# Optimization experiments

Hardware: AMD Instinct MI355X
Metric: run time of the kernel (lower is better)

Reference implementation:

```python
import jax, jax.numpy as jnp
import numpy as np

B, H, N, C = 16, 64, 128, 256
HID = 1024   # feedforward hidden
C8 = C // 8  # mlp hidden in pos/score MLPs
EPS = 1e-6


def _ln(x, g, b):
    m = jnp.mean(x, axis=-1, keepdims=True)
    v = jnp.mean((x - m) ** 2, axis=-1, keepdims=True)
    return (x - m) / jnp.sqrt(v + EPS) * g + b


def setup_inputs() -> dict:
    key = jax.random.key(0)
    ks = jax.random.split(key, 24)
    s = lambda k, shape, scale=0.05: jax.random.normal(k, shape, dtype=jnp.float32) * scale
    inp = {
        "query_input": jax.random.normal(ks[0], (B, H, C), dtype=jnp.float32),
        "key_input": jax.random.normal(ks[1], (B, H, N, C), dtype=jnp.float32),
        "relative_pos": jax.random.normal(ks[2], (B, H, N, 4), dtype=jnp.float32),
        "visibility_mask": jax.random.randint(ks[3], (B, H, N, 1), 0, 2, dtype=jnp.int32),
        # layernorms
        "ln1_g": jnp.ones((C,), jnp.float32), "ln1_b": jnp.zeros((C,), jnp.float32),
        "ln2_g": jnp.ones((C,), jnp.float32), "ln2_b": jnp.zeros((C,), jnp.float32),
        # attention projections (no bias)
        "Wq": s(ks[4], (C, C)), "Wk": s(ks[5], (C, C)), "Wv": s(ks[6], (C, C)),
        # position MLP: 4 -> C//8 -> C
        "pos_w1": s(ks[7], (4, C8)), "pos_b1": jnp.zeros((C8,), jnp.float32),
        "pos_w2": s(ks[8], (C8, C)), "pos_b2": jnp.zeros((C,), jnp.float32),
        # score MLP: C -> C//8 -> C
        "sc_w1": s(ks[9], (C, C8)), "sc_b1": jnp.zeros((C8,), jnp.float32),
        "sc_w2": s(ks[10], (C8, C)), "sc_b2": jnp.zeros((C,), jnp.float32),
        # output layer
        "Wo": s(ks[11], (C, C)), "bo": jnp.zeros((C,), jnp.float32),
        # feedforward MLP: C -> HID -> C
        "ff_w1": s(ks[12], (C, HID)), "ff_b1": jnp.zeros((HID,), jnp.float32),
        "ff_w2": s(ks[13], (HID, C)), "ff_b2": jnp.zeros((C,), jnp.float32),
    }
    return inp


def reference(query_input, key_input, relative_pos, visibility_mask,
              ln1_g, ln1_b, ln2_g, ln2_b, Wq, Wk, Wv,
              pos_w1, pos_b1, pos_w2, pos_b2,
              sc_w1, sc_b1, sc_w2, sc_b2, Wo, bo,
              ff_w1, ff_b1, ff_w2, ff_b2):
    # --- attention block with pre-norm + residual ---
    x = _ln(query_input, ln1_g, ln1_b)                      # [B,H,C]
    q = x @ Wq                                              # [B,H,C]
    k = key_input @ Wk                                      # [B,H,N,C]
    v = key_input @ Wv                                      # [B,H,N,C]
    pos = jax.nn.relu(relative_pos @ pos_w1 + pos_b1) @ pos_w2 + pos_b2  # [B,H,N,C]
    attn_in = k - q[:, :, None, :] + pos                    # [B,H,N,C]
    aw = jax.nn.relu(attn_in @ sc_w1 + sc_b1) @ sc_w2 + sc_b2  # [B,H,N,C]
    aw = jnp.where(visibility_mask == 0, -1e9, aw)
    aw = jax.nn.softmax(aw, axis=-2)                        # softmax over N
    agg = jnp.sum((v + pos) * aw, axis=2)                   # [B,H,C]
    attn_out = agg @ Wo + bo
    x = attn_out + query_input
    # --- feedforward block with pre-norm + residual ---
    y = _ln(x, ln2_g, ln2_b)
    y = jax.nn.relu(y @ ff_w1 + ff_b1) @ ff_w2 + ff_b2
    return y + x
```

## Files before the change

kernel.cpp:

```cpp
#include <hip/hip_runtime.h>
#include <math.h>

#define NN 128
#define CC 256
#define HIDN 1024
#define KST 264
#define SST 40
#define EPSL 1e-6f

typedef short s16x8 __attribute__((ext_vector_type(8)));
typedef float f32x4 __attribute__((ext_vector_type(4)));

#define WVOFF    0
#define WTOFF    73728
#define SW2OFF   82944
#define WOB_OFF  91136
#define FW1B_OFF 156672
#define FW2B_OFF 418816
#define QT_BYTE_OFF  1361920
#define AGG_BYTE_OFF 1492992

__device__ __forceinline__ unsigned short f2b(float x) {
    unsigned u = __builtin_bit_cast(unsigned, x);
    u += 0x7fffu + ((u >> 16) & 1u);
    return (unsigned short)(u >> 16);
}
__device__ __forceinline__ float b2f(unsigned short s) {
    return __builtin_bit_cast(float, ((unsigned)s) << 16);
}
__device__ __forceinline__ unsigned pack2(float a, float b) {
    return (unsigned)f2b(a) | ((unsigned)f2b(b) << 16);
}

__device__ __forceinline__ float block_sum_256(float v, float* red) {
    #pragma unroll
    for (int off = 32; off > 0; off >>= 1)
        v += __shfl_down(v, off, 64);
    const int wid = threadIdx.x >> 6;
    if ((threadIdx.x & 63) == 0) red[wid] = v;
    __syncthreads();
    float s = red[0] + red[1] + red[2] + red[3];
    __syncthreads();
    return s;
}

__global__ __launch_bounds__(256)
void prep1(const float* __restrict__ Wv, const float* __restrict__ pw2,
           const float* __restrict__ sw2, const float* __restrict__ fw1,
           const float* __restrict__ fw2, const float* __restrict__ Wo,
           unsigned short* __restrict__ ws16)
{
    int e = blockIdx.x * 256 + threadIdx.x;
    unsigned short v[8];
    if (e < 9216) {
        int koct = e >> 8, col = e & 255;
        #pragma unroll
        for (int j = 0; j < 8; ++j) {
            int k = koct * 8 + j;
            float val = (k < 256) ? Wv[k * 256 + col] : pw2[(k - 256) * 256 + col];
            v[j] = f2b(val);
        }
        int dest = WVOFF + (col >> 4) * 4608 + (koct >> 2) * 512
                 + (((((koct & 3) << 4) | (col & 15))) << 3);
        uint4 pk;
        pk.x = (unsigned)v[0] | ((unsigned)v[1] << 16);
        pk.y = (unsigned)v[2] | ((unsigned)v[3] << 16);
        pk.z = (unsigned)v[4] | ((unsigned)v[5] << 16);
        pk.w = (unsigned)v[6] | ((unsigned)v[7] << 16);
        *(uint4*)&ws16[dest] = pk;
    } else if (e < 10240) {
        int i = e - 9216;
        int koct = i & 3, col = i >> 2;
        #pragma unroll
        for (int j = 0; j < 8; ++j) v[j] = f2b(sw2[(koct * 8 + j) * 256 + col]);
        int dest = SW2OFF + (col >> 4) * 512 + ((((koct << 4) | (col & 15))) << 3);
        uint4 pk;
        pk.x = (unsigned)v[0] | ((unsigned)v[1] << 16);
        pk.y = (unsigned)v[2] | ((unsigned)v[3] << 16);
        pk.z = (unsigned)v[4] | ((unsigned)v[5] << 16);
        pk.w = (unsigned)v[6] | ((unsigned)v[7] << 16);
        *(uint4*)&ws16[dest] = pk;
    } else {
        const float* src; int base, i;
        if (e < 43008)      { src = fw1; base = FW1B_OFF; i = (e - 10240) * 8; }
        else if (e < 75776) { src = fw2; base = FW2B_OFF; i = (e - 43008) * 8; }
        else                { src = Wo;  base = WOB_OFF;  i = (e - 75776) * 8; }
        float4 a = *(const float4*)(src + i);
        float4 b = *(const float4*)(src + i + 4);
        uint4 pk;
        pk.x = pack2(a.x, a.y);
        pk.y = pack2(a.z, a.w);
        pk.z = pack2(b.x, b.y);
        pk.w = pack2(b.z, b.w);
        *(uint4*)&ws16[base + i] = pk;
    }
}

__global__ __launch_bounds__(256)
void prep2(const float* __restrict__ Wk, const float* __restrict__ pw2,
           const float* __restrict__ sw1, unsigned short* __restrict__ ws16)
{
    int tid = blockIdx.x * 256 + threadIdx.x;
    int k = tid >> 5, j = tid & 31;
    const float* row = (k < 256) ? (Wk + (size_t)k * 256) : (pw2 + (size_t)(k - 256) * 256);
    float s = 0.0f;
    for (int c = 0; c < 256; ++c) s = fmaf(row[c], sw1[c * 32 + j], s);
    int dest = WTOFF + ((j >> 4) * 9 + (k >> 5)) * 512
             + ((((((k >> 3) & 3) << 4) | (j & 15))) << 3) + (k & 7);
    ws16[dest] = f2b(s);
}

__global__ __launch_bounds__(256)
void qprep(const float* __restrict__ qin,
           const float* __restrict__ ln1g, const float* __restrict__ ln1b,
           const float* __restrict__ Wq, const float* __restrict__ pb2,
           const float* __restrict__ sw1, const float* __restrict__ sb1,
           float* __restrict__ qt)
{
    __shared__ __align__(16) float xlnL[4][CC];
    __shared__ __align__(16) float qmL[4][CC];
    const int t = threadIdx.x;
    const int lane = t & 63;
    const int r = t >> 6;
    const int b0 = blockIdx.x * 4;
    const size_t rowoff = (size_t)(b0 + r) * CC;

    float v0 = qin[rowoff + lane];
    float v1 = qin[rowoff + lane + 64];
    float v2 = qin[rowoff + lane + 128];
    float v3 = qin[rowoff + lane + 192];
    float s = v0 + v1 + v2 + v3;
    #pragma unroll
    for (int off = 32; off > 0; off >>= 1) s += __shfl_xor(s, off);
    float mean = s * (1.0f / CC);
    float d0 = v0 - mean, d1 = v1 - mean, d2 = v2 - mean, d3 = v3 - mean;
    float vs = d0 * d0 + d1 * d1 + d2 * d2 + d3 * d3;
    #pragma unroll
    for (int off = 32; off > 0; off >>= 1) vs += __shfl_xor(vs, off);
    float rstd = rsqrtf(vs * (1.0f / CC) + EPSL);
    xlnL[r][lane]       = d0 * rstd * ln1g[lane] + ln1b[lane];
    xlnL[r][lane + 64]  = d1 * rstd * ln1g[lane + 64] + ln1b[lane + 64];
    xlnL[r][lane + 128] = d2 * rstd * ln1g[lane + 128] + ln1b[lane + 128];
    xlnL[r][lane + 192] = d3 * rstd * ln1g[lane + 192] + ln1b[lane + 192];
    __syncthreads();

    float q0 = 0.f, q1 = 0.f, q2 = 0.f, q3 = 0.f;
    for (int k4 = 0; k4 < CC / 4; ++k4) {
        float4 x0 = *(const float4*)&xlnL[0][k4 * 4];
        float4 x1 = *(const float4*)&xlnL[1][k4 * 4];
        float4 x2 = *(const float4*)&xlnL[2][k4 * 4];
        float4 x3 = *(const float4*)&xlnL[3][k4 * 4];
        const float* w = Wq + (size_t)(k4 * 4) * CC + t;
        float w0 = w[0], w1 = w[CC], w2 = w[2 * CC], w3 = w[3 * CC];
        q0 = fmaf(x0.x, w0, fmaf(x0.y, w1, fmaf(x0.z, w2, fmaf(x0.w, w3, q0))));
        q1 = fmaf(x1.x, w0, fmaf(x1.y, w1, fmaf(x1.z, w2, fmaf(x1.w, w3, q1))));
        q2 = fmaf(x2.x, w0, fmaf(x2.y, w1, fmaf(x2.z, w2, fmaf(x2.w, w3, q2))));
        q3 = fmaf(x3.x, w0, fmaf(x3.y, w1, fmaf(x3.z, w2, fmaf(x3.w, w3, q3))));
    }
    float pb = pb2[t];
    qmL[0][t] = pb - q0;
    qmL[1][t] = pb - q1;
    qmL[2][t] = pb - q2;
    qmL[3][t] = pb - q3;
    __syncthreads();

    if (t < 128) {
        int r2 = t >> 5, j = t & 31;
        float acc = sb1[j];
        for (int c = 0; c < 256; ++c) acc = fmaf(qmL[r2][c], sw1[c * 32 + j], acc);
        qt[(size_t)(b0 + r2) * 32 + j] = acc;
    }
}

__global__ __launch_bounds__(256, 2)
void cft_attn(const float* __restrict__ kin, const float* __restrict__ rel,
              const int* __restrict__ vis,
              const float* __restrict__ pw1, const float* __restrict__ pb1,
              const float* __restrict__ pb2, const float* __restrict__ sb2,
              const unsigned short* __restrict__ ws16,
              const float* __restrict__ qt,
              float* __restrict__ aggout)
{
    __shared__ __align__(16) unsigned char smem[80032];
    unsigned short* keyb = (unsigned short*)smem;
    float* poolA = (float*)(smem + 77824);
    float* poolB = (float*)(smem + 78848);
    unsigned char* visb = smem + 79872;
    float* aggpool = (float*)smem;
    float* lpool   = (float*)(smem + 4096);

    const int bh = blockIdx.x;
    const int t = threadIdx.x;
    const int lane = t & 63;
    const int wvid = t >> 6;
    const int quad = lane >> 4;
    const int l16 = lane & 15;
    const int rb = wvid * 32;
    unsigned short* strip = (unsigned short*)(smem + 67584) + wvid * (32 * SST);

    const float4* kb4 = (const float4*)(kin + (size_t)bh * NN * CC);
    #pragma unroll
    for (int i = 0; i < 32; ++i) {
        int flat = i * 256 + t;
        int row = flat >> 6;
        int cu = flat & 63;
        float4 kv = kb4[flat];
        uint2 pk;
        pk.x = pack2(kv.x, kv.y);
        pk.y = pack2(kv.z, kv.w);
        *(uint2*)&keyb[row * KST + cu * 4] = pk;
    }
    if (t < NN) visb[t] = (unsigned char)(vis[(size_t)bh * NN + t] != 0);
    poolB[t] = pb2[t];

    union { s16x8 v; unsigned short u[8]; } phf0, phf1;
    {
        const int row0 = rb + l16, row1 = rb + 16 + l16;
        float4 r40 = *(const float4*)(rel + ((size_t)bh * NN + row0) * 4);
        float4 r41 = *(const float4*)(rel + ((size_t)bh * NN + row1) * 4);
        #pragma unroll
        for (int j = 0; j < 8; ++j) {
            int col = quad * 8 + j;
            float w0 = pw1[col], w1 = pw1[32 + col], w2 = pw1[64 + col], w3 = pw1[96 + col];
            float b = pb1[col];
            float v0 = fmaf(r40.x, w0, fmaf(r40.y, w1, fmaf(r40.z, w2, fmaf(r40.w, w3, b))));
            float v1 = fmaf(r41.x, w0, fmaf(r41.y, w1, fmaf(r41.z, w2, fmaf(r41.w, w3, b))));
            phf0.u[j] = f2b(fmaxf(v0, 0.0f));
            phf1.u[j] = f2b(fmaxf(v1, 0.0f));
        }
    }
    const float qt0 = qt[(size_t)bh * 32 + l16];
    const float qt1 = qt[(size_t)bh * 32 + 16 + l16];
    __syncthreads();

    const int aoff0 = (rb + l16) * KST;
    const int aoff1 = (rb + 16 + l16) * KST;
    const unsigned short* wsv = ws16 + WVOFF;
    const unsigned short* wst = ws16 + WTOFF;
    const unsigned short* ws2 = ws16 + SW2OFF;

    unsigned char vm[2][4];
    #pragma unroll
    for (int mt = 0; mt < 2; ++mt)
        #pragma unroll
        for (int r = 0; r < 4; ++r) vm[mt][r] = visb[rb + mt * 16 + quad * 4 + r];

    f32x4 hacc[2][2];
    #pragma unroll
    for (int mt = 0; mt < 2; ++mt)
        #pragma unroll
        for (int jt = 0; jt < 2; ++jt) hacc[mt][jt] = (f32x4){0.f, 0.f, 0.f, 0.f};
    #pragma unroll
    for (int kt = 0; kt < 8; ++kt) {
        s16x8 A0 = *(const s16x8*)&keyb[aoff0 + kt * 32 + quad * 8];
        s16x8 A1 = *(const s16x8*)&keyb[aoff1 + kt * 32 + quad * 8];
        #pragma unroll
        for (int jt = 0; jt < 2; ++jt) {
            s16x8 B = *(const s16x8*)(wst + (size_t)(jt * 9 + kt) * 512 + lane * 8);
            hacc[0][jt] = __builtin_amdgcn_mfma_f32_16x16x32_bf16(A0, B, hacc[0][jt], 0, 0, 0);
            hacc[1][jt] = __builtin_amdgcn_mfma_f32_16x16x32_bf16(A1, B, hacc[1][jt], 0, 0, 0);
        }
    }
    #pragma unroll
    for (int jt = 0; jt < 2; ++jt) {
        s16x8 B = *(const s16x8*)(wst + (size_t)(jt * 9 + 8) * 512 + lane * 8);
        hacc[0][jt] = __builtin_amdgcn_mfma_f32_16x16x32_bf16(phf0.v, B, hacc[0][jt], 0, 0, 0);
        hacc[1][jt] = __builtin_amdgcn_mfma_f32_16x16x32_bf16(phf1.v, B, hacc[1][jt], 0, 0, 0);
    }
    #pragma unroll
    for (int mt = 0; mt < 2; ++mt)
        #pragma unroll
        for (int jt = 0; jt < 2; ++jt) {
            float qv = jt ? qt1 : qt0;
            int rw = (mt * 16 + quad * 4) * SST + jt * 16 + l16;
            strip[rw]           = f2b(fmaxf(hacc[mt][jt][0] + qv, 0.0f));
            strip[rw + SST]     = f2b(fmaxf(hacc[mt][jt][1] + qv, 0.0f));
            strip[rw + 2 * SST] = f2b(fmaxf(hacc[mt][jt][2] + qv, 0.0f));
            strip[rw + 3 * SST] = f2b(fmaxf(hacc[mt][jt][3] + qv, 0.0f));
        }

    s16x8 H0 = *(const s16x8*)&strip[l16 * SST + quad * 8];
    s16x8 H1 = *(const s16x8*)&strip[(16 + l16) * SST + quad * 8];
    float mloc[16];
    #pragma unroll
    for (int ct = 0; ct < 16; ++ct) {
        f32x4 a0 = (f32x4){0.f, 0.f, 0.f, 0.f};
        f32x4 a1 = (f32x4){0.f, 0.f, 0.f, 0.f};
        s16x8 B = *(const s16x8*)(ws2 + ((size_t)ct * 64 + lane) * 8);
        a0 = __builtin_amdgcn_mfma_f32_16x16x32_bf16(H0, B, a0, 0, 0, 0);
        a1 = __builtin_amdgcn_mfma_f32_16x16x32_bf16(H1, B, a1, 0, 0, 0);
        float sb2c = sb2[ct * 16 + l16];
        float ml = -3.0e38f;
        #pragma unroll
        for (int r = 0; r < 4; ++r) {
            float s0 = vm[0][r] ? (a0[r] + sb2c) : -1e9f;
            float s1 = vm[1][r] ? (a1[r] + sb2c) : -1e9f;
            ml = fmaxf(ml, fmaxf(s0, s1));
        }
        ml = fmaxf(ml, __shfl_xor(ml, 16));
        ml = fmaxf(ml, __shfl_xor(ml, 32));
        mloc[ct] = ml;
    }
    __syncthreads();
    #pragma unroll 1
    for (int w = 0; w < 4; ++w) {
        if (wvid == w && lane < 16) {
            #pragma unroll
            for (int ct = 0; ct < 16; ++ct) {
                int x = ct * 16 + lane;
                poolA[x] = (w == 0) ? mloc[ct] : fmaxf(poolA[x], mloc[ct]);
            }
        }
        __syncthreads();
    }
    float Mf[16];
    #pragma unroll
    for (int ct = 0; ct < 16; ++ct) Mf[ct] = poolA[ct * 16 + l16];

    float lsp[16], aggp[16];
    #pragma unroll
    for (int ct = 0; ct < 16; ++ct) { lsp[ct] = 0.0f; aggp[ct] = 0.0f; }

    #pragma unroll 1
    for (int ck = 0; ck < 8; ++ck) {
        float ev[2][2][4];
        #pragma unroll
        for (int ctl = 0; ctl < 2; ++ctl) {
            int ct = ck * 2 + ctl;
            f32x4 a0 = (f32x4){0.f, 0.f, 0.f, 0.f};
            f32x4 a1 = (f32x4){0.f, 0.f, 0.f, 0.f};
            s16x8 B = *(const s16x8*)(ws2 + ((size_t)ct * 64 + lane) * 8);
            a0 = __builtin_amdgcn_mfma_f32_16x16x32_bf16(H0, B, a0, 0, 0, 0);
            a1 = __builtin_amdgcn_mfma_f32_16x16x32_bf16(H1, B, a1, 0, 0, 0);
            float sb2c = sb2[ct * 16 + l16];
            float M = Mf[ct];
            float ls = 0.0f;
            #pragma unroll
            for (int r = 0; r < 4; ++r) {
                float s0 = vm[0][r] ? (a0[r] + sb2c) : -1e9f;
                float s1 = vm[1][r] ? (a1[r] + sb2c) : -1e9f;
                float e0 = __expf(s0 - M);
                float e1 = __expf(s1 - M);
                ev[ctl][0][r] = e0;
                ev[ctl][1][r] = e1;
                ls += e0 + e1;
            }
            lsp[ct] = ls;
        }
        f32x4 acc[2][2];
        #pragma unroll
        for (int mt = 0; mt < 2; ++mt)
            #pragma unroll
            for (int ctl = 0; ctl < 2; ++ctl) acc[mt][ctl] = (f32x4){0.f, 0.f, 0.f, 0.f};
        #pragma unroll
        for (int kt = 0; kt < 8; ++kt) {
            s16x8 A0 = *(const s16x8*)&keyb[aoff0 + kt * 32 + quad * 8];
            s16x8 A1 = *(const s16x8*)&keyb[aoff1 + kt * 32 + quad * 8];
            #pragma unroll
            for (int ctl = 0; ctl < 2; ++ctl) {
                s16x8 B = *(const s16x8*)(wsv + ((size_t)((ck * 2 + ctl) * 9 + kt) * 512) + lane * 8);
                acc[0][ctl] = __builtin_amdgcn_mfma_f32_16x16x32_bf16(A0, B, acc[0][ctl], 0, 0, 0);
                acc[1][ctl] = __builtin_amdgcn_mfma_f32_16x16x32_bf16(A1, B, acc[1][ctl], 0, 0, 0);
            }
        }
        #pragma unroll
        for (int ctl = 0; ctl < 2; ++ctl) {
            s16x8 B = *(const s16x8*)(wsv + ((size_t)((ck * 2 + ctl) * 9 + 8) * 512) + lane * 8);
            acc[0][ctl] = __builtin_amdgcn_mfma_f32_16x16x32_bf16(phf0.v, B, acc[0][ctl], 0, 0, 0);
            acc[1][ctl] = __builtin_amdgcn_mfma_f32_16x16x32_bf16(phf1.v, B, acc[1][ctl], 0, 0, 0);
        }
        #pragma unroll
        for (int ctl = 0; ctl < 2; ++ctl) {
            const int ct = ck * 2 + ctl;
            float pb = poolB[ct * 16 + l16];
            float a = aggp[ct];
            #pragma unroll
            for (int mt = 0; mt < 2; ++mt)
                #pragma unroll
                for (int r = 0; r < 4; ++r)
                    a = fmaf(ev[ctl][mt][r], acc[mt][ctl][r] + pb, a);
            aggp[ct] = a;
        }
    }

    __syncthreads();
    #pragma unroll
    for (int ct = 0; ct < 16; ++ct) {
        float a = aggp[ct];
        a += __shfl_xor(a, 16);
        a += __shfl_xor(a, 32);
        float l = lsp[ct];
        l += __shfl_xor(l, 16);
        l += __shfl_xor(l, 32);
        if (lane < 16) {
            aggpool[wvid * 256 + ct * 16 + lane] = a;
            lpool[wvid * 256 + ct * 16 + lane] = l;
        }
    }
    __syncthreads();
    {
        float asum = aggpool[t] + aggpool[256 + t] + aggpool[512 + t] + aggpool[768 + t];
        float lsum = lpool[t] + lpool[256 + t] + lpool[512 + t] + lpool[768 + t];
        aggout[(size_t)bh * CC + t] = asum / lsum;
    }
}

__global__ __launch_bounds__(256, 2)
void cft_ffo(const float* __restrict__ aggp, const float* __restrict__ qin,
             const float* __restrict__ bo,
             const float* __restrict__ ln2g, const float* __restrict__ ln2b,
             const unsigned short* __restrict__ ws16,
             const float* __restrict__ fb1, const float* __restrict__ fb2,
             float* __restrict__ out)
{
    __shared__ __align__(16) float aggL[4][CC];
    __shared__ __align__(16) float xlnL[4][CC];
    __shared__ __align__(16) float ffh[4][HIDN];
    __shared__ float red[4];
    const int t = threadIdx.x;
    const int b0 = blockIdx.x * 4;
    const unsigned short* wob  = ws16 + WOB_OFF;
    const unsigned short* fw1b = ws16 + FW1B_OFF;
    const unsigned short* fw2b = ws16 + FW2B_OFF;

    float xq[4];
    #pragma unroll
    for (int i = 0; i < 4; ++i) {
        aggL[i][t] = aggp[(size_t)(b0 + i) * CC + t];
        xq[i] = qin[(size_t)(b0 + i) * CC + t];
    }
    __syncthreads();

    float ao[4];
    {
        float b = bo[t];
        #pragma unroll
        for (int i = 0; i < 4; ++i) ao[i] = b;
    }
    for (int k4 = 0; k4 < CC / 4; ++k4) {
        float4 a0 = *(const float4*)&aggL[0][k4 * 4];
        float4 a1 = *(const float4*)&aggL[1][k4 * 4];
        float4 a2 = *(const float4*)&aggL[2][k4 * 4];
        float4 a3 = *(const float4*)&aggL[3][k4 * 4];
        const unsigned short* w = wob + (size_t)(k4 * 4) * CC + t;
        float w0 = b2f(w[0]), w1 = b2f(w[CC]), w2 = b2f(w[2 * CC]), w3 = b2f(w[3 * CC]);
        ao[0] = fmaf(a0.x, w0, fmaf(a0.y, w1, fmaf(a0.z, w2, fmaf(a0.w, w3, ao[0]))));
        ao[1] = fmaf(a1.x, w0, fmaf(a1.y, w1, fmaf(a1.z, w2, fmaf(a1.w, w3, ao[1]))));
        ao[2] = fmaf(a2.x, w0, fmaf(a2.y, w1, fmaf(a2.z, w2, fmaf(a2.w, w3, ao[2]))));
        ao[3] = fmaf(a3.x, w0, fmaf(a3.y, w1, fmaf(a3.z, w2, fmaf(a3.w, w3, ao[3]))));
    }
    float xrs[4];
    #pragma unroll
    for (int i = 0; i < 4; ++i) xrs[i] = ao[i] + xq[i];
    __syncthreads();

    #pragma unroll
    for (int row = 0; row < 4; ++row) {
        float x = xrs[row];
        float mean = block_sum_256(x, red) * (1.0f / CC);
        float d = x - mean;
        float var = block_sum_256(d * d, red) * (1.0f / CC);
        xlnL[row][t] = d * rsqrtf(var + EPSL) * ln2g[t] + ln2b[t];
    }
    __syncthreads();
    {
        float acc[4][4];
        #pragma unroll
        for (int rr = 0; rr < 4; ++rr) {
            float b = fb1[t + 256 * rr];
            #pragma unroll
            for (int row = 0; row < 4; ++row) acc[rr][row] = b;
        }
        for (int k4 = 0; k4 < CC / 4; ++k4) {
            float4 xv[4];
            #pragma unroll
            for (int row = 0; row < 4; ++row) xv[row] = *(const float4*)&xlnL[row][k4 * 4];
            #pragma unroll
            for (int rr = 0; rr < 4; ++rr) {
                const unsigned short* w = fw1b + (size_t)(k4 * 4) * HIDN + t + 256 * rr;
                float w0 = b2f(w[0]), w1 = b2f(w[HIDN]), w2 = b2f(w[2 * HIDN]), w3 = b2f(w[3 * HIDN]);
                #pragma unroll
                for (int row = 0; row < 4; ++row)
                    acc[rr][row] = fmaf(xv[row].x, w0, fmaf(xv[row].y, w1,
                                   fmaf(xv[row].z, w2, fmaf(xv[row].w, w3, acc[rr][row]))));
            }
        }
        #pragma unroll
        for (int rr = 0; rr < 4; ++rr)
            #pragma unroll
            for (int row = 0; row < 4; ++row)
                ffh[row][t + 256 * rr] = fmaxf(acc[rr][row], 0.0f);
    }
    __syncthreads();
    {
        float o[4];
        #pragma unroll
        for (int row = 0; row < 4; ++row) o[row] = xrs[row] + fb2[t];
        for (int h4 = 0; h4 < HIDN / 4; ++h4) {
            const unsigned short* w = fw2b + (size_t)(h4 * 4) * CC + t;
            float w0 = b2f(w[0]), w1 = b2f(w[CC]), w2 = b2f(w[2 * CC]), w3 = b2f(w[3 * CC]);
            #pragma unroll
            for (int row = 0; row < 4; ++row) {
                float4 hv = *(const float4*)&ffh[row][h4 * 4];
                o[row] = fmaf(hv.x, w0, fmaf(hv.y, w1, fmaf(hv.z, w2, fmaf(hv.w, w3, o[row]))));
            }
        }
        #pragma unroll
        for (int row = 0; row < 4; ++row) out[(size_t)(b0 + row) * CC + t] = o[row];
    }
}

extern "C" void kernel_launch(void* const* d_in, const int* in_sizes, int n_in,
                              void* d_out, int out_size, void* d_ws, size_t ws_size,
                              hipStream_t stream) {
    const float* qin  = (const float*)d_in[0];
    const float* kin  = (const float*)d_in[1];
    const float* rel  = (const float*)d_in[2];
    const int*   vis  = (const int*)  d_in[3];
    const float* ln1g = (const float*)d_in[4];
    const float* ln1b = (const float*)d_in[5];
    const float* ln2g = (const float*)d_in[6];
    const float* ln2b = (const float*)d_in[7];
    const float* Wq   = (const float*)d_in[8];
    const float* Wk   = (const float*)d_in[9];
    const float* Wv   = (const float*)d_in[10];
    const float* pw1  = (const float*)d_in[11];
    const float* pb1  = (const float*)d_in[12];
    const float* pw2  = (const float*)d_in[13];
    const float* pb2  = (const float*)d_in[14];
    const float* sw1  = (const float*)d_in[15];
    const float* sb1  = (const float*)d_in[16];
    const float* sw2  = (const float*)d_in[17];
    const float* sb2  = (const float*)d_in[18];
    const float* Wo   = (const float*)d_in[19];
    const float* bo   = (const float*)d_in[20];
    const float* fw1  = (const float*)d_in[21];
    const float* fb1  = (const float*)d_in[22];
    const float* fw2  = (const float*)d_in[23];
    const float* fb2  = (const float*)d_in[24];
    (void)in_sizes; (void)n_in; (void)out_size; (void)ws_size;

    unsigned short* ws16 = (unsigned short*)d_ws;
    float* qt   = (float*)((char*)d_ws + QT_BYTE_OFF);
    float* aggb = (float*)((char*)d_ws + AGG_BYTE_OFF);
    float* o = (float*)d_out;

    prep1<<<dim3(328), dim3(256), 0, stream>>>(Wv, pw2, sw2, fw1, fw2, Wo, ws16);
    prep2<<<dim3(36), dim3(256), 0, stream>>>(Wk, pw2, sw1, ws16);
    qprep<<<dim3(256), dim3(256), 0, stream>>>(qin, ln1g, ln1b, Wq, pb2, sw1, sb1, qt);
    cft_attn<<<dim3(1024), dim3(256), 0, stream>>>(
        kin, rel, vis, pw1, pb1, pb2, sb2, ws16, qt, aggb);
    cft_ffo<<<dim3(256), dim3(256), 0, stream>>>(
        aggb, qin, bo, ln2g, ln2b, ws16, fb1, fb2, o);
}
```

Baseline: 390.4 us.

## Fold Wq into score MLP, merge prep kernels, split FFN across more blocks

Precomputes Wq·sw1 and pb2·sw1+sb1 in a single merged prep kernel, so the per-query projection becomes a 256x32 product instead of a 256x256 GEMM followed by a second reduction. It also removes one kernel launch by folding prep2 into prep1. The feed-forward kernel now handles 2 rows per block over 512 blocks, with paired bf16 weight loads and a split-K second layer reduced through shared memory. In exchange, each weight element is re-read by twice as many blocks, and bf16 rounding moves slightly because the weights are folded.

New measurement: 352.4 us. 1.11x faster.

```diff
diff --git a/kernel.cpp b/kernel.cpp
--- a/kernel.cpp
+++ b/kernel.cpp
@@ -17,8 +17,10 @@
 #define WOB_OFF  91136
 #define FW1B_OFF 156672
 #define FW2B_OFF 418816
-#define QT_BYTE_OFF  1361920
-#define AGG_BYTE_OFF 1492992
+#define QT_BYTE_OFF   1361920
+#define AGG_BYTE_OFF  1492992
+#define WQT_BYTE_OFF  2541568
+#define QTC_BYTE_OFF  2574336
 
 __device__ __forceinline__ unsigned short f2b(float x) {
     unsigned u = __builtin_bit_cast(unsigned, x);
@@ -28,6 +30,8 @@
 __device__ __forceinline__ float b2f(unsigned short s) {
     return __builtin_bit_cast(float, ((unsigned)s) << 16);
 }
+__device__ __forceinline__ float blo(unsigned u) { return b2f((unsigned short)u); }
+__device__ __forceinline__ float bhi(unsigned u) { return b2f((unsigned short)(u >> 16)); }
 __device__ __forceinline__ unsigned pack2(float a, float b) {
     return (unsigned)f2b(a) | ((unsigned)f2b(b) << 16);
 }
@@ -45,10 +49,14 @@
 }
 
 __global__ __launch_bounds__(256)
-void prep1(const float* __restrict__ Wv, const float* __restrict__ pw2,
-           const float* __restrict__ sw2, const float* __restrict__ fw1,
-           const float* __restrict__ fw2, const float* __restrict__ Wo,
-           unsigned short* __restrict__ ws16)
+void prep_all(const float* __restrict__ Wk, const float* __restrict__ Wv,
+              const float* __restrict__ Wq,
+              const float* __restrict__ pw2, const float* __restrict__ sw1,
+              const float* __restrict__ sw2, const float* __restrict__ fw1,
+              const float* __restrict__ fw2, const float* __restrict__ Wo,
+              const float* __restrict__ pb2, const float* __restrict__ sb1,
+              unsigned short* __restrict__ ws16,
+              float* __restrict__ wqt, float* __restrict__ qtc)
 {
     int e = blockIdx.x * 256 + threadIdx.x;
     unsigned short v[8];
@@ -80,7 +88,7 @@
         pk.z = (unsigned)v[4] | ((unsigned)v[5] << 16);
         pk.w = (unsigned)v[6] | ((unsigned)v[7] << 16);
         *(uint4*)&ws16[dest] = pk;
-    } else {
+    } else if (e < 83968) {
         const float* src; int base, i;
         if (e < 43008)      { src = fw1; base = FW1B_OFF; i = (e - 10240) * 8; }
         else if (e < 75776) { src = fw2; base = FW2B_OFF; i = (e - 43008) * 8; }
@@ -93,32 +101,39 @@
         pk.z = pack2(b.x, b.y);
         pk.w = pack2(b.z, b.w);
         *(uint4*)&ws16[base + i] = pk;
+    } else if (e < 93184) {
+        int tid = e - 83968;
+        int k = tid >> 5, j = tid & 31;
+        const float* row = (k < 256) ? (Wk + (size_t)k * 256) : (pw2 + (size_t)(k - 256) * 256);
+        float s = 0.0f;
+        for (int c = 0; c < 256; ++c) s = fmaf(row[c], sw1[c * 32 + j], s);
+        int dest = WTOFF + ((j >> 4) * 9 + (k >> 5)) * 512
+                 + ((((((k >> 3) & 3) << 4) | (j & 15))) << 3) + (k & 7);
+        ws16[dest] = f2b(s);
+    } else if (e < 101376) {
+        int tid = e - 93184;
+        int c = tid >> 5, j = tid & 31;
+        const float* row = Wq + (size_t)c * 256;
+        float s = 0.0f;
+        for (int cp = 0; cp < 256; ++cp) s = fmaf(row[cp], sw1[cp * 32 + j], s);
+        wqt[c * 32 + j] = s;
+    } else {
+        int j = e - 101376;
+        if (j < 32) {
+            float s = sb1[j];
+            for (int c = 0; c < 256; ++c) s = fmaf(pb2[c], sw1[c * 32 + j], s);
+            qtc[j] = s;
+        }
     }
 }
 
 __global__ __launch_bounds__(256)
-void prep2(const float* __restrict__ Wk, const float* __restrict__ pw2,
-           const float* __restrict__ sw1, unsigned short* __restrict__ ws16)
-{
-    int tid = blockIdx.x * 256 + threadIdx.x;
-    int k = tid >> 5, j = tid & 31;
-    const float* row = (k < 256) ? (Wk + (size_t)k * 256) : (pw2 + (size_t)(k - 256) * 256);
-    float s = 0.0f;
-    for (int c = 0; c < 256; ++c) s = fmaf(row[c], sw1[c * 32 + j], s);
-    int dest = WTOFF + ((j >> 4) * 9 + (k >> 5)) * 512
-             + ((((((k >> 3) & 3) << 4) | (j & 15))) << 3) + (k & 7);
-    ws16[dest] = f2b(s);
-}
-
-__global__ __launch_bounds__(256)
-void qprep(const float* __restrict__ qin,
-           const float* __restrict__ ln1g, const float* __restrict__ ln1b,
-           const float* __restrict__ Wq, const float* __restrict__ pb2,
-           const float* __restrict__ sw1, const float* __restrict__ sb1,
-           float* __restrict__ qt)
+void qprep2(const float* __restrict__ qin,
+            const float* __restrict__ ln1g, const float* __restrict__ ln1b,
+            const float* __restrict__ wqt, const float* __restrict__ qtc,
+            float* __restrict__ qt)
 {
     __shared__ __align__(16) float xlnL[4][CC];
-    __shared__ __align__(16) float qmL[4][CC];
     const int t = threadIdx.x;
     const int lane = t & 63;
     const int r = t >> 6;
@@ -144,30 +159,10 @@
     xlnL[r][lane + 192] = d3 * rstd * ln1g[lane + 192] + ln1b[lane + 192];
     __syncthreads();
 
-    float q0 = 0.f, q1 = 0.f, q2 = 0.f, q3 = 0.f;
-    for (int k4 = 0; k4 < CC / 4; ++k4) {
-        float4 x0 = *(const float4*)&xlnL[0][k4 * 4];
-        float4 x1 = *(const float4*)&xlnL[1][k4 * 4];
-        float4 x2 = *(const float4*)&xlnL[2][k4 * 4];
-        float4 x3 = *(const float4*)&xlnL[3][k4 * 4];
-        const float* w = Wq + (size_t)(k4 * 4) * CC + t;
-        float w0 = w[0], w1 = w[CC], w2 = w[2 * CC], w3 = w[3 * CC];
-        q0 = fmaf(x0.x, w0, fmaf(x0.y, w1, fmaf(x0.z, w2, fmaf(x0.w, w3, q0))));
-        q1 = fmaf(x1.x, w0, fmaf(x1.y, w1, fmaf(x1.z, w2, fmaf(x1.w, w3, q1))));
-        q2 = fmaf(x2.x, w0, fmaf(x2.y, w1, fmaf(x2.z, w2, fmaf(x2.w, w3, q2))));
-        q3 = fmaf(x3.x, w0, fmaf(x3.y, w1, fmaf(x3.z, w2, fmaf(x3.w, w3, q3))));
-    }
-    float pb = pb2[t];
-    qmL[0][t] = pb - q0;
-    qmL[1][t] = pb - q1;
-    qmL[2][t] = pb - q2;
-    qmL[3][t] = pb - q3;
-    __syncthreads();
-
     if (t < 128) {
         int r2 = t >> 5, j = t & 31;
-        float acc = sb1[j];
-        for (int c = 0; c < 256; ++c) acc = fmaf(qmL[r2][c], sw1[c * 32 + j], acc);
+        float acc = qtc[j];
+        for (int c = 0; c < 256; ++c) acc = fmaf(-xlnL[r2][c], wqt[c * 32 + j], acc);
         qt[(size_t)(b0 + r2) * 32 + j] = acc;
     }
 }
@@ -405,57 +400,47 @@
     }
 }
 
-__global__ __launch_bounds__(256, 2)
-void cft_ffo(const float* __restrict__ aggp, const float* __restrict__ qin,
-             const float* __restrict__ bo,
-             const float* __restrict__ ln2g, const float* __restrict__ ln2b,
-             const unsigned short* __restrict__ ws16,
-             const float* __restrict__ fb1, const float* __restrict__ fb2,
-             float* __restrict__ out)
+__global__ __launch_bounds__(256, 4)
+void cft_ffo2(const float* __restrict__ aggp, const float* __restrict__ qin,
+              const float* __restrict__ bo,
+              const float* __restrict__ ln2g, const float* __restrict__ ln2b,
+              const unsigned short* __restrict__ ws16,
+              const float* __restrict__ fb1, const float* __restrict__ fb2,
+              float* __restrict__ out)
 {
-    __shared__ __align__(16) float aggL[4][CC];
-    __shared__ __align__(16) float xlnL[4][CC];
-    __shared__ __align__(16) float ffh[4][HIDN];
+    __shared__ __align__(16) float aggL[2][CC];
+    __shared__ __align__(16) float xlnL[2][CC];
+    __shared__ __align__(16) float ffh[2][HIDN];
+    __shared__ __align__(16) float part[2][2][CC];
     __shared__ float red[4];
     const int t = threadIdx.x;
-    const int b0 = blockIdx.x * 4;
+    const int b0 = blockIdx.x * 2;
     const unsigned short* wob  = ws16 + WOB_OFF;
     const unsigned short* fw1b = ws16 + FW1B_OFF;
     const unsigned short* fw2b = ws16 + FW2B_OFF;
 
-    float xq[4];
-    #pragma unroll
-    for (int i = 0; i < 4; ++i) {
+    float xq[2];
+    #pragma unroll
+    for (int i = 0; i < 2; ++i) {
         aggL[i][t] = aggp[(size_t)(b0 + i) * CC + t];
         xq[i] = qin[(size_t)(b0 + i) * CC + t];
     }
     __syncthreads();
 
-    float ao[4];
-    {
-        float b = bo[t];
-        #pragma unroll
-        for (int i = 0; i < 4; ++i) ao[i] = b;
-    }
+    float ao[2];
+    { float b = bo[t]; ao[0] = b; ao[1] = b; }
     for (int k4 = 0; k4 < CC / 4; ++k4) {
         float4 a0 = *(const float4*)&aggL[0][k4 * 4];
         float4 a1 = *(const float4*)&aggL[1][k4 * 4];
-        float4 a2 = *(const float4*)&aggL[2][k4 * 4];
-        float4 a3 = *(const float4*)&aggL[3][k4 * 4];
         const unsigned short* w = wob + (size_t)(k4 * 4) * CC + t;
         float w0 = b2f(w[0]), w1 = b2f(w[CC]), w2 = b2f(w[2 * CC]), w3 = b2f(w[3 * CC]);
         ao[0] = fmaf(a0.x, w0, fmaf(a0.y, w1, fmaf(a0.z, w2, fmaf(a0.w, w3, ao[0]))));
         ao[1] = fmaf(a1.x, w0, fmaf(a1.y, w1, fmaf(a1.z, w2, fmaf(a1.w, w3, ao[1]))));
-        ao[2] = fmaf(a2.x, w0, fmaf(a2.y, w1, fmaf(a2.z, w2, fmaf(a2.w, w3, ao[2]))));
-        ao[3] = fmaf(a3.x, w0, fmaf(a3.y, w1, fmaf(a3.z, w2, fmaf(a3.w, w3, ao[3]))));
-    }
-    float xrs[4];
-    #pragma unroll
-    for (int i = 0; i < 4; ++i) xrs[i] = ao[i] + xq[i];
-    __syncthreads();
-
-    #pragma unroll
-    for (int row = 0; row < 4; ++row) {
+    }
+    float xrs[2] = { ao[0] + xq[0], ao[1] + xq[1] };
+
+    #pragma unroll
+    for (int row = 0; row < 2; ++row) {
         float x = xrs[row];
         float mean = block_sum_256(x, red) * (1.0f / CC);
         float d = x - mean;
@@ -463,51 +448,75 @@
         xlnL[row][t] = d * rsqrtf(var + EPSL) * ln2g[t] + ln2b[t];
     }
     __syncthreads();
+
     {
-        float acc[4][4];
-        #pragma unroll
-        for (int rr = 0; rr < 4; ++rr) {
-            float b = fb1[t + 256 * rr];
-            #pragma unroll
-            for (int row = 0; row < 4; ++row) acc[rr][row] = b;
-        }
+        const int h0 = 2 * t;
+        float acc[2][4];
+        acc[0][0] = acc[1][0] = fb1[h0];
+        acc[0][1] = acc[1][1] = fb1[h0 + 1];
+        acc[0][2] = acc[1][2] = fb1[h0 + 512];
+        acc[0][3] = acc[1][3] = fb1[h0 + 513];
         for (int k4 = 0; k4 < CC / 4; ++k4) {
-            float4 xv[4];
-            #pragma unroll
-            for (int row = 0; row < 4; ++row) xv[row] = *(const float4*)&xlnL[row][k4 * 4];
-            #pragma unroll
-            for (int rr = 0; rr < 4; ++rr) {
-                const unsigned short* w = fw1b + (size_t)(k4 * 4) * HIDN + t + 256 * rr;
-                float w0 = b2f(w[0]), w1 = b2f(w[HIDN]), w2 = b2f(w[2 * HIDN]), w3 = b2f(w[3 * HIDN]);
-                #pragma unroll
-                for (int row = 0; row < 4; ++row)
-                    acc[rr][row] = fmaf(xv[row].x, w0, fmaf(xv[row].y, w1,
-                                   fmaf(xv[row].z, w2, fmaf(xv[row].w, w3, acc[rr][row]))));
+            float4 x0 = *(const float4*)&xlnL[0][k4 * 4];
+            float4 x1 = *(const float4*)&xlnL[1][k4 * 4];
+            float xa0[4] = {x0.x, x0.y, x0.z, x0.w};
+            float xa1[4] = {x1.x, x1.y, x1.z, x1.w};
+            #pragma unroll
+            for (int kk = 0; kk < 4; ++kk) {
+                const int k = k4 * 4 + kk;
+                unsigned wA = *(const unsigned*)&fw1b[(size_t)k * HIDN + h0];
+                unsigned wB = *(const unsigned*)&fw1b[(size_t)k * HIDN + h0 + 512];
+                float wl = blo(wA), wh = bhi(wA), wl2 = blo(wB), wh2 = bhi(wB);
+                acc[0][0] = fmaf(xa0[kk], wl, acc[0][0]);
+                acc[0][1] = fmaf(xa0[kk], wh, acc[0][1]);
+                acc[0][2] = fmaf(xa0[kk], wl2, acc[0][2]);
+                acc[0][3] = fmaf(xa0[kk], wh2, acc[0][3]);
+                acc[1][0] = fmaf(xa1[kk], wl, acc[1][0]);
+                acc[1][1] = fmaf(xa1[kk], wh, acc[1][1]);
+                acc[1][2] = fmaf(xa1[kk], wl2, acc[1][2]);
+                acc[1][3] = fmaf(xa1[kk], wh2, acc[1][3]);
             }
         }
         #pragma unroll
-        for (int rr = 0; rr < 4; ++rr)
-            #pragma unroll
-            for (int row = 0; row < 4; ++row)
-                ffh[row][t + 256 * rr] = fmaxf(acc[rr][row], 0.0f);
-    }
-    __syncthreads();
+        for (int row = 0; row < 2; ++row) {
+            ffh[row][h0]       = fmaxf(acc[row][0], 0.0f);
+            ffh[row][h0 + 1]   = fmaxf(acc[row][1], 0.0f);
+            ffh[row][h0 + 512] = fmaxf(acc[row][2], 0.0f);
+            ffh[row][h0 + 513] = fmaxf(acc[row][3], 0.0f);
+        }
+    }
+    __syncthreads();
+
     {
-        float o[4];
-        #pragma unroll
-        for (int row = 0; row < 4; ++row) o[row] = xrs[row] + fb2[t];
-        for (int h4 = 0; h4 < HIDN / 4; ++h4) {
-            const unsigned short* w = fw2b + (size_t)(h4 * 4) * CC + t;
-            float w0 = b2f(w[0]), w1 = b2f(w[CC]), w2 = b2f(w[2 * CC]), w3 = b2f(w[3 * CC]);
-            #pragma unroll
-            for (int row = 0; row < 4; ++row) {
-                float4 hv = *(const float4*)&ffh[row][h4 * 4];
-                o[row] = fmaf(hv.x, w0, fmaf(hv.y, w1, fmaf(hv.z, w2, fmaf(hv.w, w3, o[row]))));
+        const int u = t & 127;
+        const int half = t >> 7;
+        const int c0 = 2 * u;
+        const int hbase = half * 512;
+        float oacc[2][2] = {{0.f, 0.f}, {0.f, 0.f}};
+        for (int h4 = 0; h4 < 128; ++h4) {
+            const int h = hbase + h4 * 4;
+            #pragma unroll
+            for (int hh = 0; hh < 4; ++hh) {
+                unsigned w = *(const unsigned*)&fw2b[(size_t)(h + hh) * CC + c0];
+                float w0 = blo(w), w1 = bhi(w);
+                float hv0 = ffh[0][h + hh];
+                float hv1 = ffh[1][h + hh];
+                oacc[0][0] = fmaf(hv0, w0, oacc[0][0]);
+                oacc[0][1] = fmaf(hv0, w1, oacc[0][1]);
+                oacc[1][0] = fmaf(hv1, w0, oacc[1][0]);
+                oacc[1][1] = fmaf(hv1, w1, oacc[1][1]);
             }
         }
-        #pragma unroll
-        for (int row = 0; row < 4; ++row) out[(size_t)(b0 + row) * CC + t] = o[row];
-    }
+        part[half][0][c0]     = oacc[0][0];
+        part[half][0][c0 + 1] = oacc[0][1];
+        part[half][1][c0]     = oacc[1][0];
+        part[half][1][c0 + 1] = oacc[1][1];
+    }
+    __syncthreads();
+    #pragma unroll
+    for (int row = 0; row < 2; ++row)
+        out[(size_t)(b0 + row) * CC + t] =
+            xrs[row] + fb2[t] + part[0][row][t] + part[1][row][t];
 }
 
 extern "C" void kernel_launch(void* const* d_in, const int* in_sizes, int n_in,
@@ -543,13 +552,15 @@
     unsigned short* ws16 = (unsigned short*)d_ws;
     float* qt   = (float*)((char*)d_ws + QT_BYTE_OFF);
     float* aggb = (float*)((char*)d_ws + AGG_BYTE_OFF);
+    float* wqt  = (float*)((char*)d_ws + WQT_BYTE_OFF);
+    float* qtc  = (float*)((char*)d_ws + QTC_BYTE_OFF);
     float* o = (float*)d_out;
 
-    prep1<<<dim3(328), dim3(256), 0, stream>>>(Wv, pw2, sw2, fw1, fw2, Wo, ws16);
-    prep2<<<dim3(36), dim3(256), 0, stream>>>(Wk, pw2, sw1, ws16);
-    qprep<<<dim3(256), dim3(256), 0, stream>>>(qin, ln1g, ln1b, Wq, pb2, sw1, sb1, qt);
+    prep_all<<<dim3(397), dim3(256), 0, stream>>>(
+        Wk, Wv, Wq, pw2, sw1, sw2, fw1, fw2, Wo, pb2, sb1, ws16, wqt, qtc);
+    qprep2<<<dim3(256), dim3(256), 0, stream>>>(qin, ln1g, ln1b, wqt, qtc, qt);
     cft_attn<<<dim3(1024), dim3(256), 0, stream>>>(
         kin, rel, vis, pw1, pb1, pb2, sb2, ws16, qt, aggb);
-    cft_ffo<<<dim3(256), dim3(256), 0, stream>>>(
+    cft_ffo2<<<dim3(512), dim3(256), 0, stream>>>(
         aggb, qin, bo, ln2g, ln2b, ws16, fb1, fb2, o);
 }
```
